# Kernel tuning notes

Measured on AMD Instinct MI355X. Metric: run time of the kernel, lower is better.

The kernel has to match this reference:

```python
import jax, jax.numpy as jnp
import numpy as np

B = 64; IMG = 224; P = 16; CIN = 3
DM = 192; DEPTH = 24; DSTATE = 16; DINNER = 384; DTR = 12; DCONV = 4
N = (IMG // P) ** 2  # 196 tokens


def setup_inputs() -> dict:
    key = jax.random.key(0)
    ks = jax.random.split(key, 10)
    s = 0.02
    img = jax.random.normal(ks[0], (B, CIN, IMG, IMG), jnp.float32)
    patch_w = jax.random.normal(ks[1], (DM, CIN, P, P), jnp.float32) * s
    patch_b = jnp.zeros((DM,), jnp.float32)
    # per-layer Mamba params, stacked along depth
    in_proj_w = jax.random.normal(ks[2], (DEPTH, 2 * DINNER, DM), jnp.float32) * s
    conv_w = jax.random.normal(ks[3], (DEPTH, DINNER, DCONV), jnp.float32) * s
    conv_b = jnp.zeros((DEPTH, DINNER), jnp.float32)
    x_proj_w = jax.random.normal(ks[4], (DEPTH, DTR + 2 * DSTATE, DINNER), jnp.float32) * s
    dt_w = jax.random.normal(ks[5], (DEPTH, DINNER, DTR), jnp.float32) * s
    dt_b = jax.random.normal(ks[6], (DEPTH, DINNER), jnp.float32) * s
    # S4D-real init: A = -[1..d_state]
    A_log = jnp.log(jnp.broadcast_to(jnp.arange(1, DSTATE + 1, dtype=jnp.float32), (DEPTH, DINNER, DSTATE)))
    D_param = jnp.ones((DEPTH, DINNER), jnp.float32)
    out_proj_w = jax.random.normal(ks[7], (DEPTH, DM, DINNER), jnp.float32) * s
    norm_w = jnp.ones((DM,), jnp.float32)
    norm_b = jnp.zeros((DM,), jnp.float32)
    return dict(img=img, patch_w=patch_w, patch_b=patch_b, in_proj_w=in_proj_w,
                conv_w=conv_w, conv_b=conv_b, x_proj_w=x_proj_w, dt_w=dt_w, dt_b=dt_b,
                A_log=A_log, D_param=D_param, out_proj_w=out_proj_w,
                norm_w=norm_w, norm_b=norm_b)


def _mamba(x, p):
    # x: (B, L, DM); one Mamba mixer block (mamba_ssm semantics, no residual)
    in_w, cw, cb, xpw, dtw, dtb, A_log, Dv, outw = p
    Bb, L, _ = x.shape
    xz = jnp.einsum('bld,ed->ble', x, in_w)          # (B,L,2*DINNER)
    xs, z = jnp.split(xz, 2, axis=-1)
    # causal depthwise conv1d, kernel size DCONV
    xpad = jnp.pad(xs, ((0, 0), (DCONV - 1, 0), (0, 0)))
    xc = cb + sum(xpad[:, k:k + L, :] * cw[:, k] for k in range(DCONV))
    xc = jax.nn.silu(xc)
    proj = jnp.einsum('bld,ed->ble', xc, xpw)        # (B,L,DTR+2*DSTATE)
    dt = jax.nn.softplus(jnp.einsum('blr,dr->bld', proj[..., :DTR], dtw) + dtb)  # (B,L,DINNER)
    Bm = proj[..., DTR:DTR + DSTATE]                 # (B,L,DSTATE)
    Cm = proj[..., DTR + DSTATE:]                    # (B,L,DSTATE)
    A = -jnp.exp(A_log)                              # (DINNER,DSTATE)

    def step(h, inp):
        dt_t, B_t, u_t, C_t = inp                    # (B,DINNER),(B,DSTATE),(B,DINNER),(B,DSTATE)
        dA = jnp.exp(dt_t[:, :, None] * A)
        h = h * dA + dt_t[:, :, None] * B_t[:, None, :] * u_t[:, :, None]
        y = jnp.einsum('bds,bs->bd', h, C_t)
        return h, y

    h0 = jnp.zeros((Bb, DINNER, DSTATE), x.dtype)
    _, ys = jax.lax.scan(step, h0, (dt.transpose(1, 0, 2), Bm.transpose(1, 0, 2),
                                    xc.transpose(1, 0, 2), Cm.transpose(1, 0, 2)))
    y = ys.transpose(1, 0, 2) + xc * Dv
    y = y * jax.nn.silu(z)
    return jnp.einsum('bld,od->blo', y, outw)


def _forward(img, patch_w, patch_b, in_proj_w, conv_w, conv_b, x_proj_w, dt_w, dt_b,
             A_log, D_param, out_proj_w, norm_w, norm_b):
    x = jax.lax.conv_general_dilated(img, patch_w, (P, P), 'VALID',
                                     dimension_numbers=('NCHW', 'OIHW', 'NCHW'))
    x = x + patch_b[None, :, None, None]
    x = x.reshape(x.shape[0], DM, N).transpose(0, 2, 1)  # (B,N,DM)

    def layer(c, p):
        return _mamba(c, p), None

    x, _ = jax.lax.scan(layer, x, (in_proj_w, conv_w, conv_b, x_proj_w, dt_w, dt_b,
                                   A_log, D_param, out_proj_w))
    mu = x.mean(-1, keepdims=True)
    var = ((x - mu) ** 2).mean(-1, keepdims=True)
    x = (x - mu) / jnp.sqrt(var + 1e-5) * norm_w + norm_b
    return x.mean(axis=1)  # pooled (B, DM)


def reference(img, patch_w, patch_b, in_proj_w, conv_w, conv_b, x_proj_w, dt_w, dt_b,
              A_log, D_param, out_proj_w, norm_w, norm_b):
    return _forward(img, patch_w, patch_b, in_proj_w, conv_w, conv_b, x_proj_w,
                    dt_w, dt_b, A_log, D_param, out_proj_w, norm_w, norm_b)
```

## Files before the change

kernel.cpp:

```cpp
#include <hip/hip_runtime.h>
#include <hip/hip_bf16.h>
#include <math.h>

#define BB 64
#define IMG 224
#define PP 16
#define CIN 3
#define DM 192
#define DEPTH 24
#define DSTATE 16
#define DINNER 384
#define DTR 12
#define DCONV 4
#define NP 196
#define RTOT (BB * NP)
#define CHUNKS 14
#define LC 14
#define NCMB (2 * DSTATE + DINNER)

typedef short bf16x8 __attribute__((ext_vector_type(8)));
typedef float f32x4 __attribute__((ext_vector_type(4)));

__device__ inline unsigned short f2bf_rne(float f) {
    unsigned u = __float_as_uint(f);
    unsigned r = u + 0x7fffu + ((u >> 16) & 1u);
    return (unsigned short)(r >> 16);
}
__device__ inline float bf2f(unsigned short s) {
    return __uint_as_float(((unsigned)s) << 16);
}

__global__ __launch_bounds__(256) void im2col_pack_kernel(const float* __restrict__ img,
                                                          short* __restrict__ colH) {
    size_t idx = (size_t)blockIdx.x * 256 + threadIdx.x;
    if (idx >= (size_t)RTOT * 768) return;
    int t = (int)(idx % 768);
    size_t r = idx / 768;
    int l = (int)(r % NP);
    int b = (int)(r / NP);
    int ph = l / 14, pw = l % 14;
    int ci = t / 256, rem = t % 256;
    int i = rem / 16, j = rem % 16;
    float v = img[(((size_t)b * CIN + ci) * IMG + ph * 16 + i) * IMG + pw * 16 + j];
    colH[idx] = (short)f2bf_rne(v);
}

__global__ __launch_bounds__(256) void pack_w_kernel(const float* __restrict__ W,
                                                     short* __restrict__ Wh, int NE) {
    int i = blockIdx.x * 256 + threadIdx.x;
    if (i * 4 >= NE) return;
    float4 v = *(const float4*)&W[i * 4];
    short4 h;
    h.x = (short)f2bf_rne(v.x);
    h.y = (short)f2bf_rne(v.y);
    h.z = (short)f2bf_rne(v.z);
    h.w = (short)f2bf_rne(v.w);
    *(short4*)&Wh[i * 4] = h;
}

__global__ __launch_bounds__(256) void packT_out_kernel(const float* __restrict__ outw,
                                                        short* __restrict__ wOutT) {
    int idx = blockIdx.x * 256 + threadIdx.x;
    if (idx >= DEPTH * DM * DINNER) return;
    int layer = idx / (DM * DINNER);
    int rem = idx % (DM * DINNER);
    int m = rem / DINNER;
    int k = rem % DINNER;
    float v = outw[idx];
    wOutT[((size_t)layer * DINNER + k) * DM + m] = (short)f2bf_rne(v);
}

__global__ __launch_bounds__(256) void wcmb_kernel(const float* __restrict__ xpw,
                                                   const float* __restrict__ dtw,
                                                   short* __restrict__ wCmb) {
    int idx = blockIdx.x * 256 + threadIdx.x;
    if (idx >= DEPTH * NCMB * DINNER) return;
    int layer = idx / (NCMB * DINNER);
    int rem = idx % (NCMB * DINNER);
    int n = rem / DINNER;
    int k = rem % DINNER;
    const float* xp = xpw + (size_t)layer * 44 * DINNER;
    float v;
    if (n < 32) {
        v = xp[(DTR + n) * DINNER + k];
    } else {
        int d = n - 32;
        const float* w = dtw + ((size_t)layer * DINNER + d) * DTR;
        v = 0.f;
#pragma unroll
        for (int j = 0; j < DTR; j++) v += w[j] * xp[j * DINNER + k];
    }
    wCmb[idx] = (short)f2bf_rne(v);
}

__global__ __launch_bounds__(256) void gemm_wcross_kernel(const short* __restrict__ wIn,
                                                          const short* __restrict__ wOutT,
                                                          short* __restrict__ wCross) {
    constexpr int BK = 32, LDSS = BK + 8, K = DM;
    __shared__ short As[2][64 * LDSS];
    __shared__ short Bs[2][64 * LDSS];
    const int tid = threadIdx.x;
    const int lane = tid & 63;
    const int wc = tid >> 6;
    const int layer = blockIdx.z;
    const short* Ah = wIn + ((size_t)(layer + 1)) * 768 * DM;
    const short* Bh = wOutT + (size_t)layer * DINNER * DM;
    short* Cc = wCross + (size_t)layer * 768 * DINNER;
    const int row0 = blockIdx.y * 64, col0 = blockIdx.x * 64;

    bf16x8 aPh, bPh;
    f32x4 acc[4] = {};

    auto loadG = [&](int k0) {
        int r = tid >> 2, cg = (tid & 3) * 8;
        aPh = *(const bf16x8*)&Ah[(size_t)(row0 + r) * K + k0 + cg];
        bPh = *(const bf16x8*)&Bh[(size_t)(col0 + r) * K + k0 + cg];
    };
    auto storeLDS = [&](int p) {
        int r = tid >> 2, cg = (tid & 3) * 8;
        *(bf16x8*)&As[p][r * LDSS + cg] = aPh;
        *(bf16x8*)&Bs[p][r * LDSS + cg] = bPh;
    };
    auto compute = [&](int p) {
        const int fr = lane & 15;
        const int kg = (lane >> 4) * 8;
        bf16x8 aH[4], bH;
#pragma unroll
        for (int i = 0; i < 4; i++)
            aH[i] = *(const bf16x8*)&As[p][(i * 16 + fr) * LDSS + kg];
        bH = *(const bf16x8*)&Bs[p][(wc * 16 + fr) * LDSS + kg];
#pragma unroll
        for (int i = 0; i < 4; i++)
            acc[i] = __builtin_amdgcn_mfma_f32_16x16x32_bf16(aH[i], bH, acc[i], 0, 0, 0);
    };

    loadG(0);
    storeLDS(0);
    __syncthreads();
    int p = 0;
    for (int k0 = BK;; k0 += BK) {
        const bool has_next = (k0 < K);
        if (has_next) loadG(k0);
        compute(p);
        if (!has_next) break;
        storeLDS(p ^ 1);
        __syncthreads();
        p ^= 1;
    }

    const int crow = (lane >> 4) * 4;
    const int ccol = lane & 15;
#pragma unroll
    for (int i = 0; i < 4; i++) {
        int gn = col0 + wc * 16 + ccol;
        int gm0 = row0 + i * 16 + crow;
#pragma unroll
        for (int reg = 0; reg < 4; reg++)
            Cc[(size_t)(gm0 + reg) * DINNER + gn] = (short)f2bf_rne(acc[i][reg]);
    }
}

template<int BM, int BN>
__global__ __launch_bounds__(256) void gemm_pk_kernel(const short* __restrict__ Ah,
                                                      const short* __restrict__ Bh,
                                                      float* __restrict__ C,
                                                      short* __restrict__ CBf,
                                                      const float* __restrict__ bias,
                                                      int M, int N, int K, int Kc) {
    constexpr int BK = 32;
    constexpr int LDSS = BK + 8;
    constexpr int WR = BM / 64;
    constexpr int WC = 4 / WR;
    constexpr int NJ = BN / WC / 16;
    constexpr int A8 = BM / 64;
    constexpr int B8 = BN / 64;
    __shared__ short As[2][BM * LDSS];
    __shared__ short Bs[2][BN * LDSS];

    const int tid = threadIdx.x;
    const int lane = tid & 63;
    const int wid = tid >> 6;
    const int wr = wid / WC, wc = wid % WC;
    const int row0 = blockIdx.y * BM, col0 = blockIdx.x * BN;
    const int kbase = blockIdx.z * Kc;
    const bf16x8 ZV = {0, 0, 0, 0, 0, 0, 0, 0};

    bf16x8 aPh[A8], bPh[B8];
    f32x4 acc[4][NJ] = {};

    auto loadG = [&](int k0) {
#pragma unroll
        for (int i = 0; i < A8; i++) {
            int lin = tid + i * 256;
            int r = lin >> 2, cg = (lin & 3) * 8;
            aPh[i] = *(const bf16x8*)&Ah[(size_t)(row0 + r) * K + k0 + cg];
        }
#pragma unroll
        for (int i = 0; i < B8; i++) {
            int lin = tid + i * 256;
            int r = lin >> 2, cg = (lin & 3) * 8;
            int n = col0 + r;
            bPh[i] = (n < N) ? *(const bf16x8*)&Bh[(size_t)n * K + k0 + cg] : ZV;
        }
    };
    auto storeLDS = [&](int p) {
#pragma unroll
        for (int i = 0; i < A8; i++) {
            int lin = tid + i * 256;
            int r = lin >> 2, cg = (lin & 3) * 8;
            *(bf16x8*)&As[p][r * LDSS + cg] = aPh[i];
        }
#pragma unroll
        for (int i = 0; i < B8; i++) {
            int lin = tid + i * 256;
            int r = lin >> 2, cg = (lin & 3) * 8;
            *(bf16x8*)&Bs[p][r * LDSS + cg] = bPh[i];
        }
    };
    auto compute = [&](int p) {
        const int fr = lane & 15;
        const int kg = (lane >> 4) * 8;
        bf16x8 aH[4], bH[NJ];
#pragma unroll
        for (int i = 0; i < 4; i++)
            aH[i] = *(const bf16x8*)&As[p][(wr * 64 + i * 16 + fr) * LDSS + kg];
#pragma unroll
        for (int j = 0; j < NJ; j++)
            bH[j] = *(const bf16x8*)&Bs[p][(wc * (BN / WC) + j * 16 + fr) * LDSS + kg];
#pragma unroll
        for (int i = 0; i < 4; i++)
#pragma unroll
            for (int j = 0; j < NJ; j++)
                acc[i][j] = __builtin_amdgcn_mfma_f32_16x16x32_bf16(aH[i], bH[j], acc[i][j], 0, 0, 0);
    };

    loadG(kbase);
    storeLDS(0);
    __syncthreads();
    int p = 0;
    for (int k0 = kbase + BK;; k0 += BK) {
        const bool has_next = (k0 < kbase + Kc);
        if (has_next) loadG(k0);
        compute(p);
        if (!has_next) break;
        storeLDS(p ^ 1);
        __syncthreads();
        p ^= 1;
    }

    const bool direct = (gridDim.z == 1);
    float* Cout = C + (size_t)blockIdx.z * M * N;
    const int crow = (lane >> 4) * 4;
    const int ccol = lane & 15;
#pragma unroll
    for (int i = 0; i < 4; i++)
#pragma unroll
        for (int j = 0; j < NJ; j++) {
            int gn = col0 + wc * (BN / WC) + j * 16 + ccol;
            if (gn >= N) continue;
            int gm0 = row0 + wr * 64 + i * 16 + crow;
            float bv = (direct && bias) ? bias[gn] : 0.f;
            if (direct && CBf) {
#pragma unroll
                for (int reg = 0; reg < 4; reg++)
                    CBf[(size_t)(gm0 + reg) * N + gn] = (short)f2bf_rne(acc[i][j][reg] + bv);
            } else {
#pragma unroll
                for (int reg = 0; reg < 4; reg++)
                    Cout[(size_t)(gm0 + reg) * N + gn] = acc[i][j][reg] + bv;
            }
        }
}

__global__ __launch_bounds__(256) void gemm_xproj_kernel(const short* __restrict__ Ah,
                                                         const short* __restrict__ Bh,
                                                         float* __restrict__ projBC,
                                                         short* __restrict__ dtB,
                                                         const float* __restrict__ dtb,
                                                         int M, int K) {
    constexpr int BM = 64, BN = 64, BK = 32;
    constexpr int LDSS = BK + 8;
    constexpr int N = NCMB;
    __shared__ short As[2][BM * LDSS];
    __shared__ short Bs[2][BN * LDSS];

    const int tid = threadIdx.x;
    const int lane = tid & 63;
    const int wc = tid >> 6;
    const int row0 = blockIdx.y * BM, col0 = blockIdx.x * BN;
    const bf16x8 ZV = {0, 0, 0, 0, 0, 0, 0, 0};

    bf16x8 aPh, bPh;
    f32x4 acc[4] = {};

    auto loadG = [&](int k0) {
        int r = tid >> 2, cg = (tid & 3) * 8;
        aPh = *(const bf16x8*)&Ah[(size_t)(row0 + r) * K + k0 + cg];
        int n = col0 + r;
        bPh = (n < N) ? *(const bf16x8*)&Bh[(size_t)n * K + k0 + cg] : ZV;
    };
    auto storeLDS = [&](int p) {
        int r = tid >> 2, cg = (tid & 3) * 8;
        *(bf16x8*)&As[p][r * LDSS + cg] = aPh;
        *(bf16x8*)&Bs[p][r * LDSS + cg] = bPh;
    };
    auto compute = [&](int p) {
        const int fr = lane & 15;
        const int kg = (lane >> 4) * 8;
        bf16x8 aH[4], bH;
#pragma unroll
        for (int i = 0; i < 4; i++)
            aH[i] = *(const bf16x8*)&As[p][(i * 16 + fr) * LDSS + kg];
        bH = *(const bf16x8*)&Bs[p][(wc * 16 + fr) * LDSS + kg];
#pragma unroll
        for (int i = 0; i < 4; i++)
            acc[i] = __builtin_amdgcn_mfma_f32_16x16x32_bf16(aH[i], bH, acc[i], 0, 0, 0);
    };

    loadG(0);
    storeLDS(0);
    __syncthreads();
    int p = 0;
    for (int k0 = BK;; k0 += BK) {
        const bool has_next = (k0 < K);
        if (has_next) loadG(k0);
        compute(p);
        if (!has_next) break;
        storeLDS(p ^ 1);
        __syncthreads();
        p ^= 1;
    }

    const int crow = (lane >> 4) * 4;
    const int ccol = lane & 15;
#pragma unroll
    for (int i = 0; i < 4; i++) {
        int gn = col0 + wc * 16 + ccol;
        if (gn >= NCMB) continue;
        int gm0 = row0 + i * 16 + crow;
        if (gn < 32) {
#pragma unroll
            for (int reg = 0; reg < 4; reg++)
                projBC[(size_t)(gm0 + reg) * 32 + gn] = acc[i][reg];
        } else {
            int d = gn - 32;
            float bv = dtb[d];
#pragma unroll
            for (int reg = 0; reg < 4; reg++) {
                float v = acc[i][reg] + bv;
                v = (v > 20.f) ? v : __logf(1.f + __expf(v));
                dtB[(size_t)(gm0 + reg) * DINNER + d] = (short)f2bf_rne(v);
            }
        }
    }
}

__global__ __launch_bounds__(256) void reduce_kernel(const float* __restrict__ parts,
                                                     short* __restrict__ outH,
                                                     const float* __restrict__ bias,
                                                     long MN, int N, int SK) {
    long i = (long)blockIdx.x * 256 + threadIdx.x;
    if (i * 4 >= MN) return;
    float4 acc = *(const float4*)&parts[i * 4];
    for (int z = 1; z < SK; z++) {
        float4 v = *(const float4*)&parts[(size_t)z * MN + i * 4];
        acc.x += v.x; acc.y += v.y; acc.z += v.z; acc.w += v.w;
    }
    if (bias) {
        int col = (int)((i * 4) % N);
        float4 bv = *(const float4*)&bias[col];
        acc.x += bv.x; acc.y += bv.y; acc.z += bv.z; acc.w += bv.w;
    }
    short4 h;
    h.x = (short)f2bf_rne(acc.x);
    h.y = (short)f2bf_rne(acc.y);
    h.z = (short)f2bf_rne(acc.z);
    h.w = (short)f2bf_rne(acc.w);
    *(short4*)&outH[i * 4] = h;
}

__global__ __launch_bounds__(256) void conv_silu_kernel(const short* __restrict__ xzBf,
                                                        const float* __restrict__ cw,
                                                        const float* __restrict__ cb,
                                                        short* __restrict__ xcH) {
    size_t idx = (size_t)blockIdx.x * 256 + threadIdx.x;
    if (idx >= (size_t)RTOT * (DINNER / 4)) return;
    int e0 = (int)(idx % (DINNER / 4)) * 4;
    size_t r = idx / (DINNER / 4);
    int l = (int)(r % NP);
    size_t b = r / NP;
    float acc[4];
    {
        float4 cbv = *(const float4*)&cb[e0];
        acc[0] = cbv.x; acc[1] = cbv.y; acc[2] = cbv.z; acc[3] = cbv.w;
    }
    float4 wv[4];
#pragma unroll
    for (int j = 0; j < 4; j++) wv[j] = *(const float4*)&cw[(e0 + j) * DCONV];
#pragma unroll
    for (int k = 0; k < DCONV; k++) {
        int ls = l + k - (DCONV - 1);
        if (ls >= 0) {
            short4 xv = *(const short4*)&xzBf[(b * NP + ls) * 768 + e0];
            acc[0] += bf2f((unsigned short)xv.x) * (&wv[0].x)[k];
            acc[1] += bf2f((unsigned short)xv.y) * (&wv[1].x)[k];
            acc[2] += bf2f((unsigned short)xv.z) * (&wv[2].x)[k];
            acc[3] += bf2f((unsigned short)xv.w) * (&wv[3].x)[k];
        }
    }
    short4 o;
#pragma unroll
    for (int j = 0; j < 4; j++) {
        float v = acc[j] / (1.f + __expf(-acc[j]));
        (&o.x)[j] = (short)f2bf_rne(v);
    }
    *(short4*)&xcH[r * DINNER + e0] = o;
}

__global__ __launch_bounds__(128) void scanA_kernel(const short* __restrict__ xcB,
                                                    const float* __restrict__ projBC,
                                                    const short* __restrict__ dtB,
                                                    const float* __restrict__ A_log,
                                                    short* __restrict__ hEndB,
                                                    float* __restrict__ sdtBuf) {
    int d = blockIdx.x * 128 + threadIdx.x;
    int c = blockIdx.y, b = blockIdx.z;
    float a[DSTATE], h[DSTATE];
#pragma unroll
    for (int s = 0; s < DSTATE; s++) {
        a[s] = -expf(A_log[(size_t)d * DSTATE + s]);
        h[s] = 0.f;
    }
    const float a0 = a[0];
    bool chain = true;
#pragma unroll
    for (int s = 1; s < DSTATE; s++)
        chain = chain && (fabsf(a[s] - (float)(s + 1) * a0) <= 1e-4f * fabsf(a[s]));
    float sdt = 0.f;
    size_t rbase = (size_t)b * NP + (size_t)c * LC;
    if (chain) {
        for (int l = 0; l < LC; l++) {
            size_t r = rbase + l;
            float dtv = bf2f((unsigned short)dtB[r * DINNER + d]);
            float du = dtv * bf2f((unsigned short)xcB[r * DINNER + d]);
            const float* pb = projBC + r * 32;
            float Bv[DSTATE];
            *(float4*)&Bv[0]  = *(const float4*)&pb[0];
            *(float4*)&Bv[4]  = *(const float4*)&pb[4];
            *(float4*)&Bv[8]  = *(const float4*)&pb[8];
            *(float4*)&Bv[12] = *(const float4*)&pb[12];
            float q = __expf(dtv * a0);
            float dA = q;
            h[0] = h[0] * dA + du * Bv[0];
#pragma unroll
            for (int s = 1; s < DSTATE; s++) {
                dA *= q;
                h[s] = h[s] * dA + du * Bv[s];
            }
            sdt += dtv;
        }
    } else {
        for (int l = 0; l < LC; l++) {
            size_t r = rbase + l;
            float dtv = bf2f((unsigned short)dtB[r * DINNER + d]);
            float du = dtv * bf2f((unsigned short)xcB[r * DINNER + d]);
            const float* pb = projBC + r * 32;
            float Bv[DSTATE];
            *(float4*)&Bv[0]  = *(const float4*)&pb[0];
            *(float4*)&Bv[4]  = *(const float4*)&pb[4];
            *(float4*)&Bv[8]  = *(const float4*)&pb[8];
            *(float4*)&Bv[12] = *(const float4*)&pb[12];
#pragma unroll
            for (int s = 0; s < DSTATE; s++) {
                float dA = __expf(dtv * a[s]);
                h[s] = h[s] * dA + du * Bv[s];
            }
            sdt += dtv;
        }
    }
    short* he = hEndB + (((size_t)b * CHUNKS + c) * DINNER + d) * DSTATE;
#pragma unroll
    for (int g = 0; g < 4; g++) {
        short4 o;
        o.x = (short)f2bf_rne(h[g * 4 + 0]);
        o.y = (short)f2bf_rne(h[g * 4 + 1]);
        o.z = (short)f2bf_rne(h[g * 4 + 2]);
        o.w = (short)f2bf_rne(h[g * 4 + 3]);
        *(short4*)&he[g * 4] = o;
    }
    sdtBuf[((size_t)b * CHUNKS + c) * DINNER + d] = sdt;
}

__global__ __launch_bounds__(256) void scanB_kernel(const short* __restrict__ hEndB,
                                                    const float* __restrict__ sdtBuf,
                                                    const float* __restrict__ A_log,
                                                    short* __restrict__ hInitB) {
    int idx = blockIdx.x * 256 + threadIdx.x;
    if (idx >= BB * DINNER * DSTATE) return;
    int b = idx / (DINNER * DSTATE);
    int rem = idx % (DINNER * DSTATE);
    int d = rem / DSTATE;
    int s = rem % DSTATE;
    float a = -expf(A_log[(size_t)d * DSTATE + s]);
    float run = 0.f;
    for (int c = 0; c < CHUNKS; c++) {
        size_t off = ((size_t)b * CHUNKS + c) * (DINNER * DSTATE) + rem;
        float p = __expf(a * sdtBuf[((size_t)b * CHUNKS + c) * DINNER + d]);
        float e = bf2f((unsigned short)hEndB[off]);
        hInitB[off] = (short)f2bf_rne(run);
        run = run * p + e;
    }
}

__global__ __launch_bounds__(128) void scanC_kernel(const short* __restrict__ xcB,
                                                    const float* __restrict__ projBC,
                                                    const short* __restrict__ dtB,
                                                    const short* __restrict__ hInitB,
                                                    const float* __restrict__ A_log,
                                                    const float* __restrict__ Dv,
                                                    const short* __restrict__ xzBf,
                                                    short* __restrict__ yh) {
    int d = blockIdx.x * 128 + threadIdx.x;
    int c = blockIdx.y, b = blockIdx.z;
    float a[DSTATE], h[DSTATE];
#pragma unroll
    for (int s = 0; s < DSTATE; s++)
        a[s] = -expf(A_log[(size_t)d * DSTATE + s]);
    const float a0 = a[0];
    bool chain = true;
#pragma unroll
    for (int s = 1; s < DSTATE; s++)
        chain = chain && (fabsf(a[s] - (float)(s + 1) * a0) <= 1e-4f * fabsf(a[s]));
    const short* hi = hInitB + (((size_t)b * CHUNKS + c) * DINNER + d) * DSTATE;
#pragma unroll
    for (int g = 0; g < 4; g++) {
        short4 v = *(const short4*)&hi[g * 4];
        h[g * 4 + 0] = bf2f((unsigned short)v.x);
        h[g * 4 + 1] = bf2f((unsigned short)v.y);
        h[g * 4 + 2] = bf2f((unsigned short)v.z);
        h[g * 4 + 3] = bf2f((unsigned short)v.w);
    }
    float Dd = Dv[d];
    size_t rbase = (size_t)b * NP + (size_t)c * LC;
    if (chain) {
        for (int l = 0; l < LC; l++) {
            size_t r = rbase + l;
            float dtv = bf2f((unsigned short)dtB[r * DINNER + d]);
            float u = bf2f((unsigned short)xcB[r * DINNER + d]);
            float du = dtv * u;
            const float* pb = projBC + r * 32;
            float Bv[DSTATE], Cv[DSTATE];
            *(float4*)&Bv[0]  = *(const float4*)&pb[0];
            *(float4*)&Bv[4]  = *(const float4*)&pb[4];
            *(float4*)&Bv[8]  = *(const float4*)&pb[8];
            *(float4*)&Bv[12] = *(const float4*)&pb[12];
            *(float4*)&Cv[0]  = *(const float4*)&pb[16];
            *(float4*)&Cv[4]  = *(const float4*)&pb[20];
            *(float4*)&Cv[8]  = *(const float4*)&pb[24];
            *(float4*)&Cv[12] = *(const float4*)&pb[28];
            float q = __expf(dtv * a0);
            float dA = q;
            h[0] = h[0] * dA + du * Bv[0];
            float y = h[0] * Cv[0];
#pragma unroll
            for (int s = 1; s < DSTATE; s++) {
                dA *= q;
                h[s] = h[s] * dA + du * Bv[s];
                y = fmaf(h[s], Cv[s], y);
            }
            float z = bf2f((unsigned short)xzBf[r * 768 + DINNER + d]);
            float val = (y + u * Dd) * (z / (1.f + __expf(-z)));
            yh[r * DINNER + d] = (short)f2bf_rne(val);
        }
    } else {
        for (int l = 0; l < LC; l++) {
            size_t r = rbase + l;
            float dtv = bf2f((unsigned short)dtB[r * DINNER + d]);
            float u = bf2f((unsigned short)xcB[r * DINNER + d]);
            float du = dtv * u;
            const float* pb = projBC + r * 32;
            float Bv[DSTATE], Cv[DSTATE];
            *(float4*)&Bv[0]  = *(const float4*)&pb[0];
            *(float4*)&Bv[4]  = *(const float4*)&pb[4];
            *(float4*)&Bv[8]  = *(const float4*)&pb[8];
            *(float4*)&Bv[12] = *(const float4*)&pb[12];
            *(float4*)&Cv[0]  = *(const float4*)&pb[16];
            *(float4*)&Cv[4]  = *(const float4*)&pb[20];
            *(float4*)&Cv[8]  = *(const float4*)&pb[24];
            *(float4*)&Cv[12] = *(const float4*)&pb[28];
            float y = 0.f;
#pragma unroll
            for (int s = 0; s < DSTATE; s++) {
                float dA = __expf(dtv * a[s]);
                h[s] = h[s] * dA + du * Bv[s];
                y = fmaf(h[s], Cv[s], y);
            }
            float z = bf2f((unsigned short)xzBf[r * 768 + DINNER + d]);
            float val = (y + u * Dd) * (z / (1.f + __expf(-z)));
            yh[r * DINNER + d] = (short)f2bf_rne(val);
        }
    }
}

__global__ __launch_bounds__(256) void ln_stats_kernel(const short* __restrict__ xh,
                                                       float* __restrict__ stats) {
    int r = blockIdx.x * 4 + (threadIdx.x >> 6);
    int lane = threadIdx.x & 63;
    if (r >= RTOT) return;
    float s = 0.f, ss = 0.f;
    for (int c = lane; c < DM; c += 64) {
        float v = bf2f((unsigned short)xh[(size_t)r * DM + c]);
        s += v;
        ss += v * v;
    }
#pragma unroll
    for (int o = 32; o > 0; o >>= 1) {
        s += __shfl_down(s, o);
        ss += __shfl_down(ss, o);
    }
    if (lane == 0) {
        float mu = s / (float)DM;
        float var = ss / (float)DM - mu * mu;
        stats[r * 2] = mu;
        stats[r * 2 + 1] = rsqrtf(var + 1e-5f);
    }
}

__global__ __launch_bounds__(256) void ln_mean_kernel(const short* __restrict__ xh,
                                                      const float* __restrict__ stats,
                                                      const float* __restrict__ nw,
                                                      const float* __restrict__ nb,
                                                      float* __restrict__ out) {
    int idx = blockIdx.x * 256 + threadIdx.x;
    if (idx >= BB * DM) return;
    int c = idx % DM;
    int b = idx / DM;
    float acc = 0.f;
    for (int l = 0; l < NP; l++) {
        size_t r = (size_t)b * NP + l;
        float v = bf2f((unsigned short)xh[r * DM + c]);
        acc += (v - stats[r * 2]) * stats[r * 2 + 1];
    }
    out[idx] = acc * (1.f / (float)NP) * nw[c] + nb[c];
}

extern "C" void kernel_launch(void* const* d_in, const int* in_sizes, int n_in,
                              void* d_out, int out_size, void* d_ws, size_t ws_size,
                              hipStream_t stream) {
    const float* img     = (const float*)d_in[0];
    const float* patch_w = (const float*)d_in[1];
    const float* patch_b = (const float*)d_in[2];
    const float* in_w    = (const float*)d_in[3];
    const float* conv_w  = (const float*)d_in[4];
    const float* conv_b  = (const float*)d_in[5];
    const float* xpw     = (const float*)d_in[6];
    const float* dtw     = (const float*)d_in[7];
    const float* dtb     = (const float*)d_in[8];
    const float* A_log   = (const float*)d_in[9];
    const float* Dv      = (const float*)d_in[10];
    const float* outw    = (const float*)d_in[11];
    const float* norm_w  = (const float*)d_in[12];
    const float* norm_b  = (const float*)d_in[13];
    float* out = (float*)d_out;

    float* ws = (float*)d_ws;
    const size_t R = RTOT;
    const size_t SCN = (size_t)BB * CHUNKS * DINNER * DSTATE;
    const size_t PLY = R * DINNER;

    float* xA      = ws;
    float* xB      = xA + R * DM / 2;
    float* xzB     = xB + R * DM / 2;
    float* xcB     = xzB + R * 768 / 2;
    float* dtBf    = xcB + R * DINNER / 2;
    float* projBC  = dtBf + R * DINNER / 2;
    float* scratch = projBC + R * 32;
    float* wAll    = scratch + 2 * SCN;
    float* wCrossF = wAll + 4644864;
    float* stats   = wCrossF + 3391488;

    short* wPatch = (short*)wAll;
    short* wIn    = wPatch + (size_t)DM * 768;
    short* wOut   = wIn + (size_t)DEPTH * 2 * DINNER * DM;
    short* wCmb   = wOut + (size_t)DEPTH * DM * DINNER;
    short* wCross = (short*)wCrossF;

    short* hEndB  = (short*)scratch;
    short* hInitB = hEndB + SCN;
    float* sdtBuf = scratch + SCN;
    short* y2h    = (short*)(sdtBuf + (size_t)BB * CHUNKS * DINNER);
    short* wOutT  = (short*)scratch;

    pack_w_kernel<<<dim3((DM * 768 / 4 + 255) / 256), 256, 0, stream>>>(
        patch_w, wPatch, DM * 768);
    pack_w_kernel<<<dim3((DEPTH * 2 * DINNER * DM / 4 + 255) / 256), 256, 0, stream>>>(
        in_w, wIn, DEPTH * 2 * DINNER * DM);
    pack_w_kernel<<<dim3((DEPTH * DM * DINNER / 4 + 255) / 256), 256, 0, stream>>>(
        outw, wOut, DEPTH * DM * DINNER);
    wcmb_kernel<<<dim3((DEPTH * NCMB * DINNER + 255) / 256), 256, 0, stream>>>(
        xpw, dtw, wCmb);
    packT_out_kernel<<<dim3((DEPTH * DM * DINNER + 255) / 256), 256, 0, stream>>>(
        outw, wOutT);
    gemm_wcross_kernel<<<dim3(DINNER / 64, 768 / 64, DEPTH - 1), 256, 0, stream>>>(
        wIn, wOutT, wCross);

    {
        short* colH = (short*)xzB;
        size_t n = R * 768;
        im2col_pack_kernel<<<dim3((unsigned)((n + 255) / 256)), 256, 0, stream>>>(img, colH);
        gemm_pk_kernel<64, 64><<<dim3(3, RTOT / 64, 4), 256, 0, stream>>>(
            colH, wPatch, scratch, nullptr, nullptr, RTOT, DM, 768, 192);
        long MN = (long)RTOT * DM;
        reduce_kernel<<<dim3((unsigned)((MN / 4 + 255) / 256)), 256, 0, stream>>>(
            scratch, (short*)xA, patch_b, MN, DM, 4);
    }

    short* xzH = (short*)xzB;
    short* xcH = (short*)xcB;
    short* dtH = (short*)dtBf;

    gemm_pk_kernel<64, 128><<<dim3(768 / 128, RTOT / 64, 1), 256, 0, stream>>>(
        (short*)xA, wIn, nullptr, xzH, nullptr, RTOT, 2 * DINNER, DM, DM);

    for (int layer = 0; layer < DEPTH; layer++) {
        const float* conv_wl = conv_w + (size_t)layer * DINNER * DCONV;
        const float* conv_bl = conv_b + (size_t)layer * DINNER;
        const float* dtb_l   = dtb + (size_t)layer * DINNER;
        const float* Alog_l  = A_log + (size_t)layer * DINNER * DSTATE;
        const float* Dv_l    = Dv + (size_t)layer * DINNER;
        short* wCmb_l = wCmb + (size_t)layer * NCMB * DINNER;

        {
            size_t n = R * (DINNER / 4);
            conv_silu_kernel<<<dim3((unsigned)((n + 255) / 256)), 256, 0, stream>>>(
                xzH, conv_wl, conv_bl, xcH);
        }
        gemm_xproj_kernel<<<dim3(7, RTOT / 64), 256, 0, stream>>>(
            xcH, wCmb_l, projBC, dtH, dtb_l, RTOT, DINNER);
        scanA_kernel<<<dim3(3, CHUNKS, BB), 128, 0, stream>>>(
            xcH, projBC, dtH, Alog_l, hEndB, sdtBuf);
        scanB_kernel<<<dim3((BB * DINNER * DSTATE + 255) / 256), 256, 0, stream>>>(
            hEndB, sdtBuf, Alog_l, hInitB);
        scanC_kernel<<<dim3(3, CHUNKS, BB), 128, 0, stream>>>(
            xcH, projBC, dtH, hInitB, Alog_l, Dv_l, xzH, y2h);
        if (layer < DEPTH - 1) {
            short* wX = wCross + (size_t)layer * 768 * DINNER;
            gemm_pk_kernel<64, 128><<<dim3(768 / 128, RTOT / 64, 1), 256, 0, stream>>>(
                y2h, wX, nullptr, xzH, nullptr, RTOT, 2 * DINNER, DINNER, DINNER);
        } else {
            short* wOut_l = wOut + (size_t)layer * DM * DINNER;
            gemm_pk_kernel<64, 64><<<dim3(DM / 64, RTOT / 64, 1), 256, 0, stream>>>(
                y2h, wOut_l, nullptr, (short*)xB, nullptr, RTOT, DM, DINNER, DINNER);
        }
    }

    short* xfH = (short*)xB;
    ln_stats_kernel<<<dim3(RTOT / 4), 256, 0, stream>>>(xfH, stats);
    ln_mean_kernel<<<dim3((BB * DM + 255) / 256), 256, 0, stream>>>(
        xfH, stats, norm_w, norm_b, out);
}
```

Before: 2.568 ms.

## Fold inter-chunk state propagation into scanC, removing scanB kernel

```diff
diff --git a/kernel.cpp b/kernel.cpp
--- a/kernel.cpp
+++ b/kernel.cpp
@@ -491,31 +491,11 @@
     sdtBuf[((size_t)b * CHUNKS + c) * DINNER + d] = sdt;
 }
 
-__global__ __launch_bounds__(256) void scanB_kernel(const short* __restrict__ hEndB,
-                                                    const float* __restrict__ sdtBuf,
-                                                    const float* __restrict__ A_log,
-                                                    short* __restrict__ hInitB) {
-    int idx = blockIdx.x * 256 + threadIdx.x;
-    if (idx >= BB * DINNER * DSTATE) return;
-    int b = idx / (DINNER * DSTATE);
-    int rem = idx % (DINNER * DSTATE);
-    int d = rem / DSTATE;
-    int s = rem % DSTATE;
-    float a = -expf(A_log[(size_t)d * DSTATE + s]);
-    float run = 0.f;
-    for (int c = 0; c < CHUNKS; c++) {
-        size_t off = ((size_t)b * CHUNKS + c) * (DINNER * DSTATE) + rem;
-        float p = __expf(a * sdtBuf[((size_t)b * CHUNKS + c) * DINNER + d]);
-        float e = bf2f((unsigned short)hEndB[off]);
-        hInitB[off] = (short)f2bf_rne(run);
-        run = run * p + e;
-    }
-}
-
 __global__ __launch_bounds__(128) void scanC_kernel(const short* __restrict__ xcB,
                                                     const float* __restrict__ projBC,
                                                     const short* __restrict__ dtB,
-                                                    const short* __restrict__ hInitB,
+                                                    const short* __restrict__ hEndB,
+                                                    const float* __restrict__ sdtBuf,
                                                     const float* __restrict__ A_log,
                                                     const float* __restrict__ Dv,
                                                     const short* __restrict__ xzBf,
@@ -524,22 +504,46 @@
     int c = blockIdx.y, b = blockIdx.z;
     float a[DSTATE], h[DSTATE];
 #pragma unroll
-    for (int s = 0; s < DSTATE; s++)
+    for (int s = 0; s < DSTATE; s++) {
         a[s] = -expf(A_log[(size_t)d * DSTATE + s]);
+        h[s] = 0.f;
+    }
     const float a0 = a[0];
     bool chain = true;
 #pragma unroll
     for (int s = 1; s < DSTATE; s++)
         chain = chain && (fabsf(a[s] - (float)(s + 1) * a0) <= 1e-4f * fabsf(a[s]));
-    const short* hi = hInitB + (((size_t)b * CHUNKS + c) * DINNER + d) * DSTATE;
-#pragma unroll
-    for (int g = 0; g < 4; g++) {
-        short4 v = *(const short4*)&hi[g * 4];
-        h[g * 4 + 0] = bf2f((unsigned short)v.x);
-        h[g * 4 + 1] = bf2f((unsigned short)v.y);
-        h[g * 4 + 2] = bf2f((unsigned short)v.z);
-        h[g * 4 + 3] = bf2f((unsigned short)v.w);
-    }
+
+    for (int cc = 0; cc < c; cc++) {
+        float sd = sdtBuf[((size_t)b * CHUNKS + cc) * DINNER + d];
+        const short* he = hEndB + (((size_t)b * CHUNKS + cc) * DINNER + d) * DSTATE;
+        float e[DSTATE];
+#pragma unroll
+        for (int g = 0; g < 4; g++) {
+            short4 v = *(const short4*)&he[g * 4];
+            e[g * 4 + 0] = bf2f((unsigned short)v.x);
+            e[g * 4 + 1] = bf2f((unsigned short)v.y);
+            e[g * 4 + 2] = bf2f((unsigned short)v.z);
+            e[g * 4 + 3] = bf2f((unsigned short)v.w);
+        }
+        if (chain) {
+            float q = __expf(a0 * sd);
+            float pp = q;
+            h[0] = h[0] * pp + e[0];
+#pragma unroll
+            for (int s = 1; s < DSTATE; s++) {
+                pp *= q;
+                h[s] = h[s] * pp + e[s];
+            }
+        } else {
+#pragma unroll
+            for (int s = 0; s < DSTATE; s++) {
+                float pp = __expf(a[s] * sd);
+                h[s] = h[s] * pp + e[s];
+            }
+        }
+    }
+
     float Dd = Dv[d];
     size_t rbase = (size_t)b * NP + (size_t)c * LC;
     if (chain) {
@@ -686,7 +690,6 @@
     short* wCross = (short*)wCrossF;
 
     short* hEndB  = (short*)scratch;
-    short* hInitB = hEndB + SCN;
     float* sdtBuf = scratch + SCN;
     short* y2h    = (short*)(sdtBuf + (size_t)BB * CHUNKS * DINNER);
     short* wOutT  = (short*)scratch;
@@ -739,10 +742,8 @@
             xcH, wCmb_l, projBC, dtH, dtb_l, RTOT, DINNER);
         scanA_kernel<<<dim3(3, CHUNKS, BB), 128, 0, stream>>>(
             xcH, projBC, dtH, Alog_l, hEndB, sdtBuf);
-        scanB_kernel<<<dim3((BB * DINNER * DSTATE + 255) / 256), 256, 0, stream>>>(
-            hEndB, sdtBuf, Alog_l, hInitB);
         scanC_kernel<<<dim3(3, CHUNKS, BB), 128, 0, stream>>>(
-            xcH, projBC, dtH, hInitB, Alog_l, Dv_l, xzH, y2h);
+            xcH, projBC, dtH, hEndB, sdtBuf, Alog_l, Dv_l, xzH, y2h);
         if (layer < DEPTH - 1) {
             short* wX = wCross + (size_t)layer * 768 * DINNER;
             gemm_pk_kernel<64, 128><<<dim3(768 / 128, RTOT / 64, 1), 256, 0, stream>>>(
```

Result: slower. 2.629 ms (+2.4%).
